# Kernel optimization log

Hardware: AMD Instinct MI355X
Metric: run time of the kernel (lower is better)

The kernel has to match this reference:

```python
import jax, jax.numpy as jnp
import numpy as np

G = 2.0  # gamma divergence parameter (obj='importance', g != 1.0 -> log_g path)

def setup_inputs() -> dict:
    key = jax.random.key(0)
    ks = jax.random.split(key, 6)
    V, H, N, K = 250000, 128, 32768, 256
    weight = jax.random.normal(ks[0], (V, H), dtype=jnp.float32) * 0.02
    bias = jax.random.normal(ks[1], (V,), dtype=jnp.float32) * 0.02
    hiddens = jax.random.normal(ks[2], (N, H), dtype=jnp.float32)
    # Categorical(noise).logits: normalized log-probabilities over the vocab
    noise_logits = jax.nn.log_softmax(jax.random.normal(ks[3], (V,), dtype=jnp.float32))
    targets = jax.random.randint(ks[4], (N,), 0, V, dtype=jnp.int64)
    samples = jax.random.randint(ks[5], (K,), 0, V, dtype=jnp.int64)
    return {"weight": weight, "bias": bias, "hiddens": hiddens,
            "noise_logits": noise_logits, "targets": targets, "samples": samples}

def reference(weight, bias, hiddens, noise_logits, targets, samples):
    N = hiddens.shape[0]
    K = samples.shape[0]
    # target score: <h_i, w_{t_i}> + b_{t_i}  -> [N]
    target_model = jnp.sum(hiddens * weight[targets], axis=1) + bias[targets]
    # noise scores: small gathered-weight GEMM -> [N, K]
    noise_model = hiddens @ weight[samples].T + bias[samples]
    model_logits = jnp.concatenate([target_model[:, None], noise_model], axis=1)  # [N, K+1]
    noise_l = jnp.concatenate(
        [noise_logits[targets][:, None],
         jnp.broadcast_to(noise_logits[samples][None, :], (N, K))], axis=1)
    output = model_logits - noise_l  # [N, K+1]
    # log_g: logits - log(sum(exp(g*logits)))/g, computed stably via logsumexp
    res0 = output[:, 0] - jax.nn.logsumexp(G * output, axis=1) / G  # new_targets are all 0
    return -jnp.sum(res0) / N
```

## Files before the change

kernel.cpp:

```cpp
#include <hip/hip_runtime.h>
#include <hip/hip_bf16.h>

typedef unsigned short u16;
typedef __attribute__((ext_vector_type(4))) float f32x4;
typedef __attribute__((ext_vector_type(8))) short bf16x8;

#define HDIM 128

__device__ __forceinline__ short f2b(float x) {
  union { __hip_bfloat16 b; short s; } u;
  u.b = __float2bfloat16(x);
  return u.s;
}

__global__ void prep_kernel(const float* __restrict__ weight,
                            const float* __restrict__ bias,
                            const float* __restrict__ nlog,
                            const int* __restrict__ samples,
                            u16* __restrict__ wsb,
                            float* __restrict__ ck2,
                            float* __restrict__ acc) {
  const int k = blockIdx.x;
  const int s = samples[k];
  wsb[k * HDIM + threadIdx.x] =
      (u16)f2b(2.0f * weight[(size_t)s * HDIM + threadIdx.x]);
  if (threadIdx.x == 0) {
    ck2[k] = 2.0f * (bias[s] - nlog[s]);
    if (k == 0) acc[0] = 0.0f;
  }
}

__launch_bounds__(256, 4)
__global__ void loss_kernel(const float* __restrict__ hiddens,
                            const float* __restrict__ weight,
                            const float* __restrict__ bias,
                            const float* __restrict__ nlog,
                            const int* __restrict__ targets,
                            const u16* __restrict__ wsb,
                            const float* __restrict__ ck2,
                            float* __restrict__ acc) {
  const int tid  = threadIdx.x;
  const int lane = tid & 63;
  const int wave = tid >> 6;
  const int m    = lane & 15;
  const int quad = lane >> 4;
  const int row  = blockIdx.x * 64 + wave * 16 + m;

  const float* __restrict__ hrow = hiddens + (size_t)row * HDIM;

  const int tgt = targets[row];
  const float* __restrict__ trow = weight + (size_t)tgt * HDIM;
  float p = 0.0f;
#pragma unroll
  for (int j = 0; j < 8; ++j) {
    const float4 hv = *reinterpret_cast<const float4*>(hrow + quad * 32 + j * 4);
    const float4 wv = *reinterpret_cast<const float4*>(trow + quad * 32 + j * 4);
    p += hv.x * wv.x + hv.y * wv.y + hv.z * wv.z + hv.w * wv.w;
  }
  p += __shfl_xor(p, 16);
  p += __shfl_xor(p, 32);
  const float y0 = 2.0f * (p + bias[tgt] - nlog[tgt]);

  float y0r[4];
#pragma unroll
  for (int r = 0; r < 4; ++r) y0r[r] = __shfl(y0, quad * 4 + r);

  bf16x8 af[4];
#pragma unroll
  for (int kq = 0; kq < 4; ++kq) {
    const float4 f0 = *reinterpret_cast<const float4*>(hrow + kq * 32 + quad * 8);
    const float4 f1 = *reinterpret_cast<const float4*>(hrow + kq * 32 + quad * 8 + 4);
    bf16x8 a;
    a[0] = f2b(f0.x); a[1] = f2b(f0.y); a[2] = f2b(f0.z); a[3] = f2b(f0.w);
    a[4] = f2b(f1.x); a[5] = f2b(f1.y); a[6] = f2b(f1.z); a[7] = f2b(f1.w);
    af[kq] = a;
  }

  float s0 = 0.f, s1 = 0.f, s2 = 0.f, s3 = 0.f;
#pragma unroll 4
  for (int ct = 0; ct < 16; ++ct) {
    const int col = ct * 16 + m;
    const u16* __restrict__ bp = wsb + (size_t)col * HDIM;
    f32x4 c = {0.f, 0.f, 0.f, 0.f};
#pragma unroll
    for (int kq = 0; kq < 4; ++kq) {
      const bf16x8 bf = *reinterpret_cast<const bf16x8*>(bp + kq * 32 + quad * 8);
      c = __builtin_amdgcn_mfma_f32_16x16x32_bf16(af[kq], bf, c, 0, 0, 0);
    }
    const float e = ck2[col];
    s0 += __expf(c[0] + e - y0r[0]);
    s1 += __expf(c[1] + e - y0r[1]);
    s2 += __expf(c[2] + e - y0r[2]);
    s3 += __expf(c[3] + e - y0r[3]);
  }

#pragma unroll
  for (int d = 1; d < 16; d <<= 1) {
    s0 += __shfl_xor(s0, d);
    s1 += __shfl_xor(s1, d);
    s2 += __shfl_xor(s2, d);
    s3 += __shfl_xor(s3, d);
  }
  float part = __logf(1.0f + s0) + __logf(1.0f + s1) +
               __logf(1.0f + s2) + __logf(1.0f + s3);
  part *= -0.5f;
  part += __shfl_xor(part, 16);
  part += __shfl_xor(part, 32);
  if (lane == 0) atomicAdd(acc, part);
}

__global__ void finish_kernel(const float* __restrict__ acc,
                              float* __restrict__ out, float scale) {
  out[0] = acc[0] * scale;
}

extern "C" void kernel_launch(void* const* d_in, const int* in_sizes, int n_in,
                              void* d_out, int out_size, void* d_ws, size_t ws_size,
                              hipStream_t stream) {
  const float* weight  = (const float*)d_in[0];
  const float* bias    = (const float*)d_in[1];
  const float* hiddens = (const float*)d_in[2];
  const float* nlog    = (const float*)d_in[3];
  const int*   targets = (const int*)d_in[4];
  const int*   samples = (const int*)d_in[5];
  const int N = in_sizes[2] / HDIM;
  const int K = in_sizes[5];

  u16*   wsb = (u16*)d_ws;
  float* ck2 = (float*)((char*)d_ws + (size_t)K * HDIM * sizeof(u16));
  float* acc = ck2 + K;

  prep_kernel<<<K, HDIM, 0, stream>>>(weight, bias, nlog, samples, wsb, ck2, acc);
  loss_kernel<<<N / 64, 256, 0, stream>>>(hiddens, weight, bias, nlog, targets,
                                          wsb, ck2, acc);
  finish_kernel<<<1, 1, 0, stream>>>(acc, (float*)d_out, -1.0f / (float)N);
}
```

Measured before the change: 222.4 us.

## Fuse finish kernel into loss kernel via last-block ticket and vectorize prep

Removes the separate single-thread finish kernel by having the last block to finish (tracked with an atomic ticket counter) write the scaled result. Per-block partials are combined in shared memory so only one atomic per block hits the global accumulator instead of one per wave. The prep kernel processes eight samples per 256-thread block with float4 loads and 8-byte stores. This trades a kernel launch and some atomic traffic for an extra counter atomic and a threadfence per block.

Result: faster. 209.4 us (-5.8%).

```diff
diff --git a/kernel.cpp b/kernel.cpp
--- a/kernel.cpp
+++ b/kernel.cpp
@@ -19,15 +19,17 @@
                             const int* __restrict__ samples,
                             u16* __restrict__ wsb,
                             float* __restrict__ ck2,
-                            float* __restrict__ acc) {
-  const int k = blockIdx.x;
+                            float* __restrict__ acc,
+                            int* __restrict__ cnt) {
+  const int k = blockIdx.x * 8 + (threadIdx.x >> 5);
+  const int h = (threadIdx.x & 31) * 4;
   const int s = samples[k];
-  wsb[k * HDIM + threadIdx.x] =
-      (u16)f2b(2.0f * weight[(size_t)s * HDIM + threadIdx.x]);
-  if (threadIdx.x == 0) {
-    ck2[k] = 2.0f * (bias[s] - nlog[s]);
-    if (k == 0) acc[0] = 0.0f;
-  }
+  const float4 w = *reinterpret_cast<const float4*>(weight + (size_t)s * HDIM + h);
+  u16 o[4] = {(u16)f2b(2.0f * w.x), (u16)f2b(2.0f * w.y),
+              (u16)f2b(2.0f * w.z), (u16)f2b(2.0f * w.w)};
+  *reinterpret_cast<ulong1*>(wsb + (size_t)k * HDIM + h) = *reinterpret_cast<ulong1*>(o);
+  if ((threadIdx.x & 31) == 0) ck2[k] = 2.0f * (bias[s] - nlog[s]);
+  if (threadIdx.x == 0 && blockIdx.x == 0) { acc[0] = 0.0f; cnt[0] = 0; }
 }
 
 __launch_bounds__(256, 4)
@@ -38,7 +40,11 @@
                             const int* __restrict__ targets,
                             const u16* __restrict__ wsb,
                             const float* __restrict__ ck2,
-                            float* __restrict__ acc) {
+                            float* __restrict__ acc,
+                            int* __restrict__ cnt,
+                            float* __restrict__ out,
+                            float scale) {
+  __shared__ float bsum[4];
   const int tid  = threadIdx.x;
   const int lane = tid & 63;
   const int wave = tid >> 6;
@@ -106,12 +112,18 @@
   part *= -0.5f;
   part += __shfl_xor(part, 16);
   part += __shfl_xor(part, 32);
-  if (lane == 0) atomicAdd(acc, part);
-}
+  if (lane == 0) bsum[wave] = part;
+  __syncthreads();
 
-__global__ void finish_kernel(const float* __restrict__ acc,
-                              float* __restrict__ out, float scale) {
-  out[0] = acc[0] * scale;
+  if (tid == 0) {
+    atomicAdd(acc, bsum[0] + bsum[1] + bsum[2] + bsum[3]);
+    __threadfence();
+    const int ticket = atomicAdd(cnt, 1);
+    if (ticket == (int)gridDim.x - 1) {
+      const float total = atomicAdd(acc, 0.0f);
+      out[0] = total * scale;
+    }
+  }
 }
 
 extern "C" void kernel_launch(void* const* d_in, const int* in_sizes, int n_in,
@@ -129,9 +141,11 @@
   u16*   wsb = (u16*)d_ws;
   float* ck2 = (float*)((char*)d_ws + (size_t)K * HDIM * sizeof(u16));
   float* acc = ck2 + K;
+  int*   cnt = (int*)(acc + 1);
 
-  prep_kernel<<<K, HDIM, 0, stream>>>(weight, bias, nlog, samples, wsb, ck2, acc);
+  prep_kernel<<<K / 8, 256, 0, stream>>>(weight, bias, nlog, samples, wsb, ck2,
+                                         acc, cnt);
   loss_kernel<<<N / 64, 256, 0, stream>>>(hiddens, weight, bias, nlog, targets,
-                                          wsb, ck2, acc);
-  finish_kernel<<<1, 1, 0, stream>>>(acc, (float*)d_out, -1.0f / (float)N);
+                                          wsb, ck2, acc, cnt, (float*)d_out,
+                                          -1.0f / (float)N);
 }
```
